# Kernel optimization log

Hardware: AMD Instinct MI355X
Metric: run time of the kernel (lower is better)

## Reference

```python
import jax, jax.numpy as jnp
import numpy as np

# model dims
C_CH = 64      # channels C
M_DIM = 128    # state dim m
R = 8          # low-rank r
DG = 64        # token_dim d_g
CHUNK = 512    # chunk_len
B, H, W = 4, 256, 256


def setup_inputs() -> dict:
    key = jax.random.key(0)
    ks = jax.random.split(key, 12)
    n = jax.random.normal
    return {
        "x": n(ks[0], (B, C_CH, H, W), jnp.float32),
        "g": n(ks[1], (B, DG), jnp.float32),
        # 1x1 conv weights flattened to matrices
        "in_proj_w": n(ks[2], (M_DIM, C_CH), jnp.float32) * 0.05,
        "in_proj_b": jnp.zeros((M_DIM,), jnp.float32),
        "out_proj_w": n(ks[3], (C_CH, M_DIM), jnp.float32) * 0.05,  # Cbase; conv bias unused in forward
        "U_base": n(ks[4], (M_DIM, R), jnp.float32) * 0.02,
        "V_base": n(ks[5], (M_DIM, R), jnp.float32) * 0.02,
        "a_base": jnp.zeros((M_DIM,), jnp.float32),
        "mod_uv_w": n(ks[6], (2 * R, DG), jnp.float32) * 0.05,
        "mod_uv_b": jnp.zeros((2 * R,), jnp.float32),
        "mod_a_w": n(ks[7], (M_DIM, DG), jnp.float32) * 0.05,
        "mod_a_b": jnp.zeros((M_DIM,), jnp.float32),
        "mod_B_w": n(ks[8], (M_DIM, DG), jnp.float32) * 0.05,
        "mod_B_b": jnp.zeros((M_DIM,), jnp.float32),
        "mod_C_w": n(ks[9], (C_CH, DG), jnp.float32) * 0.05,
        "mod_C_b": jnp.zeros((C_CH,), jnp.float32),
        "h0": jnp.zeros((M_DIM,), jnp.float32),
    }


def reference(x, g, in_proj_w, in_proj_b, out_proj_w, U_base, V_base, a_base,
              mod_uv_w, mod_uv_b, mod_a_w, mod_a_b, mod_B_w, mod_B_b,
              mod_C_w, mod_C_b, h0):
    Bsz, Cch, Hh, Ww = x.shape
    # 1x1 conv in_proj
    x_proj = jnp.einsum('bchw,mc->bmhw', x, in_proj_w) + in_proj_b[None, :, None, None]
    # g-conditioned modulations
    uv = g @ mod_uv_w.T + mod_uv_b
    gU = jnp.clip(uv[:, :R], -0.5, 0.5)[:, None, :]          # (B,1,r)
    gV = jnp.clip(uv[:, R:], -0.5, 0.5)[:, None, :]          # (B,1,r)
    ga = jnp.clip(g @ mod_a_w.T + mod_a_b, -2.0, 2.0)        # (B,m)
    gB = jnp.clip(g @ mod_B_w.T + mod_B_b, -1.0, 1.0)        # (B,m)
    gC = jnp.clip(g @ mod_C_w.T + mod_C_b, -0.5, 0.5)        # (B,C)
    Ug = U_base[None] * (1.0 + gU)                            # (B,m,r)
    Vg = V_base[None] * (1.0 + gV)                            # (B,m,r)
    a = a_base[None] + ga                                     # (B,m)
    Cg = out_proj_w[None] * (1.0 + gC)[:, :, None]            # (B,C,m)

    L = Hh * Ww
    x_seq = x_proj.reshape(Bsz, M_DIM, L).transpose(0, 2, 1)  # (B,L,m)
    x_seq = x_seq * (1.0 + gB)[:, None, :]
    pad = (-L) % CHUNK
    if pad > 0:
        x_seq = jnp.pad(x_seq, ((0, 0), (0, pad), (0, 0)))
    Lp = L + pad
    Mch = Lp // CHUNK
    # (T, B, K, m): scan over time within chunks, chunks run in parallel
    x_chunks = x_seq.reshape(Bsz, Mch, CHUNK, M_DIM).transpose(2, 0, 1, 3)
    h_init = jnp.broadcast_to(h0, (Bsz, Mch, M_DIM))

    def step(h, xt):
        v = jnp.einsum('bmr,bkm->bkr', Vg, h)                 # V^T h
        Av = jnp.einsum('bmr,bkr->bkm', Ug, v)                # U (V^T h)
        h_new = jnp.clip(Av + h * a[:, None, :] + xt, -10.0, 10.0)
        yc = jnp.clip(jnp.einsum('bcm,bkm->bkc', Cg, h_new), -10.0, 10.0)
        return h_new, yc

    _, ys = jax.lax.scan(step, h_init, x_chunks)              # (T,B,K,C)
    out_flat = ys.transpose(1, 2, 0, 3).reshape(Bsz, Lp, Cch)[:, :L, :]
    return out_flat.transpose(0, 2, 1).reshape(Bsz, Cch, Hh, Ww)
```

## Files before the change

### kernel.cpp

```cpp
#include <hip/hip_runtime.h>
#include <hip/hip_fp16.h>

#define L_TOT 65536

#define WS_UG   0
#define WS_VG   4096
#define WS_A    8192
#define WS_GB1  8704
#define WS_WHP  12288
#define WS_WLP  16384
#define WS_CGP  32768
#define WS_XS   65536

typedef __attribute__((ext_vector_type(8))) short short8;
typedef __attribute__((ext_vector_type(4))) float f32x4;

__device__ __forceinline__ unsigned bf16rne(float f) {
    unsigned u = __builtin_bit_cast(unsigned, f);
    return (u + 0x7fffu + ((u >> 16) & 1u)) >> 16;
}
__device__ __forceinline__ float bfhi(unsigned u) {
    return __builtin_bit_cast(float, u << 16);
}

#define DPP_ROW(CT) \
    "v_add_f32_dpp %0, %0, %0 " CT "\n\t" \
    "v_add_f32_dpp %1, %1, %1 " CT "\n\t" \
    "v_add_f32_dpp %2, %2, %2 " CT "\n\t" \
    "v_add_f32_dpp %3, %3, %3 " CT "\n\t" \
    "v_add_f32_dpp %4, %4, %4 " CT "\n\t" \
    "v_add_f32_dpp %5, %5, %5 " CT "\n\t" \
    "v_add_f32_dpp %6, %6, %6 " CT "\n\t" \
    "v_add_f32_dpp %7, %7, %7 " CT "\n\t"

__global__ __launch_bounds__(128) void mod_kernel(
    const float* __restrict__ g, const float* __restrict__ in_proj_w,
    const float* __restrict__ U_base, const float* __restrict__ V_base,
    const float* __restrict__ a_base, const float* __restrict__ out_proj_w,
    const float* __restrict__ mod_uv_w, const float* __restrict__ mod_uv_b,
    const float* __restrict__ mod_a_w, const float* __restrict__ mod_a_b,
    const float* __restrict__ mod_B_w, const float* __restrict__ mod_B_b,
    const float* __restrict__ mod_C_w, const float* __restrict__ mod_C_b,
    float* __restrict__ ws)
{
    __shared__ float gsh[64];
    __shared__ float uvs[16];
    __shared__ float gCs[64];
    const int b = blockIdx.x, tid = threadIdx.x;
    if (tid < 64) gsh[tid] = g[b * 64 + tid];
    __syncthreads();
    if (tid < 16) {
        float s = mod_uv_b[tid];
        for (int d = 0; d < 64; ++d) s += mod_uv_w[tid * 64 + d] * gsh[d];
        uvs[tid] = fminf(0.5f, fmaxf(-0.5f, s));
    }
    float ga_v, gB_v;
    {
        float s = mod_a_b[tid];
        for (int d = 0; d < 64; ++d) s += mod_a_w[tid * 64 + d] * gsh[d];
        ga_v = fminf(2.0f, fmaxf(-2.0f, s));
    }
    {
        float s = mod_B_b[tid];
        for (int d = 0; d < 64; ++d) s += mod_B_w[tid * 64 + d] * gsh[d];
        gB_v = 1.0f + fminf(1.0f, fmaxf(-1.0f, s));
    }
    if (tid < 64) {
        float s = mod_C_b[tid];
        for (int d = 0; d < 64; ++d) s += mod_C_w[tid * 64 + d] * gsh[d];
        gCs[tid] = 1.0f + fminf(0.5f, fmaxf(-0.5f, s));
    }
    __syncthreads();
    for (int idx = tid; idx < 1024; idx += 128) {
        int m = idx >> 3, r = idx & 7;
        ws[WS_UG + (b * 128 + m) * 8 + r] = U_base[m * 8 + r] * (1.0f + uvs[r]);
        ws[WS_VG + (b * 128 + m) * 8 + r] = V_base[m * 8 + r] * (1.0f + uvs[8 + r]);
    }
    ws[WS_A   + b * 128 + tid] = a_base[tid] + ga_v;
    ws[WS_GB1 + b * 128 + tid] = gB_v;
    unsigned* CgP = (unsigned*)(ws + WS_CGP);
    for (int idx = tid; idx < 4096; idx += 128) {
        int c = idx >> 6, j = idx & 63;
        float s = gCs[c];
        float c0 = out_proj_w[c * 128 + 2 * j]     * s;
        float c1 = out_proj_w[c * 128 + 2 * j + 1] * s;
        CgP[(b * 64 + c) * 64 + j] = bf16rne(c0) | (bf16rne(c1) << 16);
    }
    if (b == 0) {
        unsigned* WhP = (unsigned*)(ws + WS_WHP);
        unsigned* WlP = (unsigned*)(ws + WS_WLP);
        for (int idx = tid; idx < 4096; idx += 128) {
            int m = idx >> 5, j = idx & 31;
            float w0 = in_proj_w[m * 64 + 2 * j];
            float w1 = in_proj_w[m * 64 + 2 * j + 1];
            unsigned u0 = bf16rne(w0), u1 = bf16rne(w1);
            WhP[idx] = u0 | (u1 << 16);
            float r0 = w0 - bfhi(u0);
            float r1 = w1 - bfhi(u1);
            WlP[idx] = bf16rne(r0) | (bf16rne(r1) << 16);
        }
    }
}

__global__ __launch_bounds__(256) void inproj_mfma(
    const float* __restrict__ x, const unsigned* __restrict__ WhP,
    const unsigned* __restrict__ WlP, const float* __restrict__ bias,
    const float* __restrict__ ws, unsigned* __restrict__ xs16)
{
    __shared__ __align__(16) unsigned XhS[64 * 36];
    __shared__ __align__(16) unsigned XlS[64 * 36];
    const int tid = threadIdx.x;
    const int b = blockIdx.y;
    const int l0 = blockIdx.x * 64;

    {
        const int l_st = tid & 63, cpg = tid >> 6;
        #pragma unroll
        for (int s = 0; s < 8; ++s) {
            int cp = cpg * 8 + s;
            float x0 = x[(size_t)(b * 64 + 2 * cp) * L_TOT + l0 + l_st];
            float x1 = x[(size_t)(b * 64 + 2 * cp + 1) * L_TOT + l0 + l_st];
            unsigned u0 = bf16rne(x0), u1 = bf16rne(x1);
            XhS[l_st * 36 + cp] = u0 | (u1 << 16);
            float r0 = x0 - bfhi(u0);
            float r1 = x1 - bfhi(u1);
            XlS[l_st * 36 + cp] = bf16rne(r0) | (bf16rne(r1) << 16);
        }
    }
    const int lane = tid & 63, wv = tid >> 6;
    const int row16 = lane & 15, grp = lane >> 4;

    short8 Ah[2][2], Al[2][2];
    #pragma unroll
    for (int t = 0; t < 2; ++t) {
        const int mrow = (2 * wv + t) * 16 + row16;
        #pragma unroll
        for (int kc = 0; kc < 2; ++kc) {
            Ah[t][kc] = __builtin_bit_cast(short8,
                *(const uint4*)(WhP + mrow * 32 + kc * 16 + grp * 4));
            Al[t][kc] = __builtin_bit_cast(short8,
                *(const uint4*)(WlP + mrow * 32 + kc * 16 + grp * 4));
        }
    }
    __syncthreads();

    #pragma unroll
    for (int ti = 0; ti < 4; ++ti) {
        const int lcol = ti * 16 + row16;
        short8 Bh[2], Bl[2];
        #pragma unroll
        for (int kc = 0; kc < 2; ++kc) {
            Bh[kc] = __builtin_bit_cast(short8,
                *(const uint4*)&XhS[lcol * 36 + kc * 16 + grp * 4]);
            Bl[kc] = __builtin_bit_cast(short8,
                *(const uint4*)&XlS[lcol * 36 + kc * 16 + grp * 4]);
        }
        #pragma unroll
        for (int t = 0; t < 2; ++t) {
            f32x4 acc = {0.f, 0.f, 0.f, 0.f};
            acc = __builtin_amdgcn_mfma_f32_16x16x32_bf16(Ah[t][0], Bh[0], acc, 0, 0, 0);
            acc = __builtin_amdgcn_mfma_f32_16x16x32_bf16(Ah[t][1], Bh[1], acc, 0, 0, 0);
            acc = __builtin_amdgcn_mfma_f32_16x16x32_bf16(Ah[t][0], Bl[0], acc, 0, 0, 0);
            acc = __builtin_amdgcn_mfma_f32_16x16x32_bf16(Ah[t][1], Bl[1], acc, 0, 0, 0);
            acc = __builtin_amdgcn_mfma_f32_16x16x32_bf16(Al[t][0], Bh[0], acc, 0, 0, 0);
            acc = __builtin_amdgcn_mfma_f32_16x16x32_bf16(Al[t][1], Bh[1], acc, 0, 0, 0);
            const int mb = (2 * wv + t) * 16 + 4 * grp;
            const int l = l0 + lcol;
            float4 bi = *(const float4*)(bias + mb);
            float4 gb = *(const float4*)(ws + WS_GB1 + b * 128 + mb);
            float v0 = (acc[0] + bi.x) * gb.x;
            float v1 = (acc[1] + bi.y) * gb.y;
            float v2 = (acc[2] + bi.z) * gb.z;
            float v3 = (acc[3] + bi.w) * gb.w;
            __half2 h01 = __floats2half2_rn(v0, v1);
            __half2 h23 = __floats2half2_rn(v2, v3);
            uint2 pk = {__builtin_bit_cast(unsigned, h01), __builtin_bit_cast(unsigned, h23)};
            *(uint2*)(xs16 + ((size_t)b * L_TOT + l) * 64 + (mb >> 1)) = pk;
        }
    }
}

__global__ __launch_bounds__(64, 1) void scan_kernel(
    const unsigned* __restrict__ xs16, const float* __restrict__ ws,
    const unsigned* __restrict__ CgP, const float* __restrict__ h0,
    float* __restrict__ out)
{
    __shared__ __align__(16) unsigned Hs[16 * 68];
    const int lane = threadIdx.x;
    const int bb = blockIdx.x >> 7, k = blockIdx.x & 127;
    const int m0 = 2 * lane;

    float Vg0[8], Vg1[8], Ug0[8], Ug1[8];
    {
        const float* vg = ws + WS_VG + (bb * 128 + m0) * 8;
        const float* ug = ws + WS_UG + (bb * 128 + m0) * 8;
        #pragma unroll
        for (int r = 0; r < 8; ++r) {
            Vg0[r] = vg[r]; Vg1[r] = vg[8 + r];
            Ug0[r] = ug[r]; Ug1[r] = ug[8 + r];
        }
    }
    const float a0 = ws[WS_A + bb * 128 + m0];
    const float a1 = ws[WS_A + bb * 128 + m0 + 1];
    float ha = h0[m0], hb = h0[m0 + 1];

    short8 Af[4][4];
    const int row16 = lane & 15, grp = lane >> 4;
    #pragma unroll
    for (int ct = 0; ct < 4; ++ct)
        #pragma unroll
        for (int kc = 0; kc < 4; ++kc) {
            const unsigned* p = CgP + (bb * 64 + ct * 16 + row16) * 64 + kc * 16 + grp * 4;
            Af[ct][kc] = __builtin_bit_cast(short8, *(const uint4*)p);
        }

    const unsigned* xsp = xs16 + ((size_t)bb * L_TOT + (size_t)k * 512) * 64 + lane;
    float* ob[4];
    #pragma unroll
    for (int ct = 0; ct < 4; ++ct)
        ob[ct] = out + (size_t)(bb * 64 + ct * 16 + grp * 4) * L_TOT + k * 512 + row16;

    unsigned xqA[16], xqB[16];

    auto prefetch = [&](unsigned (&xq)[16], int seg) {
        const unsigned* xb = xsp + (size_t)seg * 1024;
        #pragma unroll
        for (int i = 0; i < 16; ++i) xq[i] = xb[(size_t)i * 64];
    };
    auto do_seg = [&](const unsigned (&xq)[16], int t16) {
        #pragma unroll
        for (int i = 0; i < 16; ++i) {
            const float2 xv = __half22float2(__builtin_bit_cast(__half2, xq[i]));
            float p0 = fmaf(Vg1[0], hb, Vg0[0] * ha);
            float p1 = fmaf(Vg1[1], hb, Vg0[1] * ha);
            float p2 = fmaf(Vg1[2], hb, Vg0[2] * ha);
            float p3 = fmaf(Vg1[3], hb, Vg0[3] * ha);
            float p4 = fmaf(Vg1[4], hb, Vg0[4] * ha);
            float p5 = fmaf(Vg1[5], hb, Vg0[5] * ha);
            float p6 = fmaf(Vg1[6], hb, Vg0[6] * ha);
            float p7 = fmaf(Vg1[7], hb, Vg0[7] * ha);
            asm volatile(
                "s_nop 1\n\t"
                DPP_ROW("quad_perm:[1,0,3,2] row_mask:0xf bank_mask:0xf bound_ctrl:1")
                DPP_ROW("quad_perm:[2,3,0,1] row_mask:0xf bank_mask:0xf bound_ctrl:1")
                DPP_ROW("row_half_mirror row_mask:0xf bank_mask:0xf bound_ctrl:1")
                DPP_ROW("row_mirror row_mask:0xf bank_mask:0xf bound_ctrl:1")
                DPP_ROW("row_bcast:15 row_mask:0xa bank_mask:0xf")
                DPP_ROW("row_bcast:31 row_mask:0xc bank_mask:0xf")
                : "+v"(p0), "+v"(p1), "+v"(p2), "+v"(p3),
                  "+v"(p4), "+v"(p5), "+v"(p6), "+v"(p7));
            float v0 = __builtin_bit_cast(float, __builtin_amdgcn_readlane(__builtin_bit_cast(int, p0), 63));
            float v1 = __builtin_bit_cast(float, __builtin_amdgcn_readlane(__builtin_bit_cast(int, p1), 63));
            float v2 = __builtin_bit_cast(float, __builtin_amdgcn_readlane(__builtin_bit_cast(int, p2), 63));
            float v3 = __builtin_bit_cast(float, __builtin_amdgcn_readlane(__builtin_bit_cast(int, p3), 63));
            float v4 = __builtin_bit_cast(float, __builtin_amdgcn_readlane(__builtin_bit_cast(int, p4), 63));
            float v5 = __builtin_bit_cast(float, __builtin_amdgcn_readlane(__builtin_bit_cast(int, p5), 63));
            float v6 = __builtin_bit_cast(float, __builtin_amdgcn_readlane(__builtin_bit_cast(int, p6), 63));
            float v7 = __builtin_bit_cast(float, __builtin_amdgcn_readlane(__builtin_bit_cast(int, p7), 63));
            float q0 = fmaf(v1, Ug0[1], v0 * Ug0[0]);
            float q1 = fmaf(v3, Ug0[3], v2 * Ug0[2]);
            float q2 = fmaf(v5, Ug0[5], v4 * Ug0[4]);
            float q3 = fmaf(v7, Ug0[7], v6 * Ug0[6]);
            float av0 = (q0 + q1) + (q2 + q3);
            float s0 = fmaf(v1, Ug1[1], v0 * Ug1[0]);
            float s1 = fmaf(v3, Ug1[3], v2 * Ug1[2]);
            float s2 = fmaf(v5, Ug1[5], v4 * Ug1[4]);
            float s3 = fmaf(v7, Ug1[7], v6 * Ug1[6]);
            float av1 = (s0 + s1) + (s2 + s3);
            ha = fminf(10.0f, fmaxf(-10.0f, fmaf(a0, ha, av0) + xv.x));
            hb = fminf(10.0f, fmaxf(-10.0f, fmaf(a1, hb, av1) + xv.y));
            unsigned hp;
            asm("v_cvt_pk_bf16_f32 %0, %1, %2" : "=v"(hp) : "v"(ha), "v"(hb));
            Hs[i * 68 + lane] = hp;
        }
        short8 Bf[4];
        #pragma unroll
        for (int kc = 0; kc < 4; ++kc)
            Bf[kc] = __builtin_bit_cast(short8,
                *(const uint4*)&Hs[row16 * 68 + kc * 16 + grp * 4]);
        #pragma unroll
        for (int ct = 0; ct < 4; ++ct) {
            f32x4 acc = {0.0f, 0.0f, 0.0f, 0.0f};
            #pragma unroll
            for (int kc = 0; kc < 4; ++kc)
                acc = __builtin_amdgcn_mfma_f32_16x16x32_bf16(Af[ct][kc], Bf[kc], acc, 0, 0, 0);
            #pragma unroll
            for (int r = 0; r < 4; ++r) {
                float y = fminf(10.0f, fmaxf(-10.0f, acc[r]));
                ob[ct][(size_t)r * L_TOT + t16 * 16] = y;
            }
        }
    };

    prefetch(xqA, 0);
    #pragma unroll 1
    for (int t16 = 0; t16 < 32; t16 += 2) {
        prefetch(xqB, t16 + 1);
        do_seg(xqA, t16);
        prefetch(xqA, (t16 + 2) & 31);
        do_seg(xqB, t16 + 1);
    }
}

extern "C" void kernel_launch(void* const* d_in, const int* in_sizes, int n_in,
                              void* d_out, int out_size, void* d_ws, size_t ws_size,
                              hipStream_t stream) {
    const float* x          = (const float*)d_in[0];
    const float* g          = (const float*)d_in[1];
    const float* in_proj_w  = (const float*)d_in[2];
    const float* in_proj_b  = (const float*)d_in[3];
    const float* out_proj_w = (const float*)d_in[4];
    const float* U_base     = (const float*)d_in[5];
    const float* V_base     = (const float*)d_in[6];
    const float* a_base     = (const float*)d_in[7];
    const float* mod_uv_w   = (const float*)d_in[8];
    const float* mod_uv_b   = (const float*)d_in[9];
    const float* mod_a_w    = (const float*)d_in[10];
    const float* mod_a_b    = (const float*)d_in[11];
    const float* mod_B_w    = (const float*)d_in[12];
    const float* mod_B_b    = (const float*)d_in[13];
    const float* mod_C_w    = (const float*)d_in[14];
    const float* mod_C_b    = (const float*)d_in[15];
    const float* h0         = (const float*)d_in[16];
    float* out = (float*)d_out;
    float* ws  = (float*)d_ws;
    unsigned* xs16 = (unsigned*)(ws + WS_XS);

    hipLaunchKernelGGL(mod_kernel, dim3(4), dim3(128), 0, stream,
                       g, in_proj_w, U_base, V_base, a_base, out_proj_w,
                       mod_uv_w, mod_uv_b, mod_a_w, mod_a_b,
                       mod_B_w, mod_B_b, mod_C_w, mod_C_b, ws);
    hipLaunchKernelGGL(inproj_mfma, dim3(1024, 4), dim3(256), 0, stream,
                       x, (const unsigned*)(ws + WS_WHP), (const unsigned*)(ws + WS_WLP),
                       in_proj_b, ws, xs16);
    hipLaunchKernelGGL(scan_kernel, dim3(512), dim3(64), 0, stream,
                       xs16, ws, (const unsigned*)(ws + WS_CGP), h0, out);
}
```

Before: 172.1 us.

## Restructure scan V^T h reduction with transposed DPP butterfly and switch output MFMA to fp16

The per-step reduction of V^T h is reorganised. The eight partial vectors are first combined across lanes, with each lane holding an xor-permuted slice of V and U, so a single register carries the rank components. That register is then summed across the wave with a swizzle and shuffle, and its values are redistributed via DPP instead of using six DPP stages per vector plus eight readlanes. The aim is to shorten the serial dependency chain of the recurrence, which bounds latency. Separately, the output-projection MFMA and the packing of Cg and H move from bf16 to fp16, which gains mantissa precision but has less range headroom (h is clipped to ±10, so this is fine).

```diff
diff --git a/kernel.cpp b/kernel.cpp
--- a/kernel.cpp
+++ b/kernel.cpp
@@ -14,6 +14,7 @@
 
 typedef __attribute__((ext_vector_type(8))) short short8;
 typedef __attribute__((ext_vector_type(4))) float f32x4;
+typedef _Float16 half8 __attribute__((ext_vector_type(8)));
 
 __device__ __forceinline__ unsigned bf16rne(float f) {
     unsigned u = __builtin_bit_cast(unsigned, f);
@@ -22,16 +23,10 @@
 __device__ __forceinline__ float bfhi(unsigned u) {
     return __builtin_bit_cast(float, u << 16);
 }
-
-#define DPP_ROW(CT) \
-    "v_add_f32_dpp %0, %0, %0 " CT "\n\t" \
-    "v_add_f32_dpp %1, %1, %1 " CT "\n\t" \
-    "v_add_f32_dpp %2, %2, %2 " CT "\n\t" \
-    "v_add_f32_dpp %3, %3, %3 " CT "\n\t" \
-    "v_add_f32_dpp %4, %4, %4 " CT "\n\t" \
-    "v_add_f32_dpp %5, %5, %5 " CT "\n\t" \
-    "v_add_f32_dpp %6, %6, %6 " CT "\n\t" \
-    "v_add_f32_dpp %7, %7, %7 " CT "\n\t"
+__device__ __forceinline__ unsigned f16pk(float a, float b) {
+    __half2 h = __floats2half2_rn(a, b);
+    return __builtin_bit_cast(unsigned, h);
+}
 
 __global__ __launch_bounds__(128) void mod_kernel(
     const float* __restrict__ g, const float* __restrict__ in_proj_w,
@@ -84,7 +79,7 @@
         float s = gCs[c];
         float c0 = out_proj_w[c * 128 + 2 * j]     * s;
         float c1 = out_proj_w[c * 128 + 2 * j + 1] * s;
-        CgP[(b * 64 + c) * 64 + j] = bf16rne(c0) | (bf16rne(c1) << 16);
+        CgP[(b * 64 + c) * 64 + j] = f16pk(c0, c1);
     }
     if (b == 0) {
         unsigned* WhP = (unsigned*)(ws + WS_WHP);
@@ -172,9 +167,7 @@
             float v1 = (acc[1] + bi.y) * gb.y;
             float v2 = (acc[2] + bi.z) * gb.z;
             float v3 = (acc[3] + bi.w) * gb.w;
-            __half2 h01 = __floats2half2_rn(v0, v1);
-            __half2 h23 = __floats2half2_rn(v2, v3);
-            uint2 pk = {__builtin_bit_cast(unsigned, h01), __builtin_bit_cast(unsigned, h23)};
+            uint2 pk = {f16pk(v0, v1), f16pk(v2, v3)};
             *(uint2*)(xs16 + ((size_t)b * L_TOT + l) * 64 + (mb >> 1)) = pk;
         }
     }
@@ -189,29 +182,31 @@
     const int lane = threadIdx.x;
     const int bb = blockIdx.x >> 7, k = blockIdx.x & 127;
     const int m0 = 2 * lane;
-
-    float Vg0[8], Vg1[8], Ug0[8], Ug1[8];
+    const int lp = lane & 7;
+    const int row16 = lane & 15, grp = lane >> 4;
+
+    float VgP0[8], VgP1[8], U0x[8], U1x[8];
     {
         const float* vg = ws + WS_VG + (bb * 128 + m0) * 8;
         const float* ug = ws + WS_UG + (bb * 128 + m0) * 8;
         #pragma unroll
-        for (int r = 0; r < 8; ++r) {
-            Vg0[r] = vg[r]; Vg1[r] = vg[8 + r];
-            Ug0[r] = ug[r]; Ug1[r] = ug[8 + r];
+        for (int j = 0; j < 8; ++j) {
+            int r = j ^ lp;
+            VgP0[j] = vg[r];     VgP1[j] = vg[8 + r];
+            U0x[j]  = ug[r];     U1x[j]  = ug[8 + r];
         }
     }
     const float a0 = ws[WS_A + bb * 128 + m0];
     const float a1 = ws[WS_A + bb * 128 + m0 + 1];
     float ha = h0[m0], hb = h0[m0 + 1];
 
-    short8 Af[4][4];
-    const int row16 = lane & 15, grp = lane >> 4;
+    half8 Af[4][4];
     #pragma unroll
     for (int ct = 0; ct < 4; ++ct)
         #pragma unroll
         for (int kc = 0; kc < 4; ++kc) {
             const unsigned* p = CgP + (bb * 64 + ct * 16 + row16) * 64 + kc * 16 + grp * 4;
-            Af[ct][kc] = __builtin_bit_cast(short8, *(const uint4*)p);
+            Af[ct][kc] = __builtin_bit_cast(half8, *(const uint4*)p);
         }
 
     const unsigned* xsp = xs16 + ((size_t)bb * L_TOT + (size_t)k * 512) * 64 + lane;
@@ -221,69 +216,89 @@
         ob[ct] = out + (size_t)(bb * 64 + ct * 16 + grp * 4) * L_TOT + k * 512 + row16;
 
     unsigned xqA[16], xqB[16];
-
     auto prefetch = [&](unsigned (&xq)[16], int seg) {
         const unsigned* xb = xsp + (size_t)seg * 1024;
         #pragma unroll
         for (int i = 0; i < 16; ++i) xq[i] = xb[(size_t)i * 64];
     };
+
+    const float fz = 0.0f;
+
     auto do_seg = [&](const unsigned (&xq)[16], int t16) {
         #pragma unroll
         for (int i = 0; i < 16; ++i) {
             const float2 xv = __half22float2(__builtin_bit_cast(__half2, xq[i]));
-            float p0 = fmaf(Vg1[0], hb, Vg0[0] * ha);
-            float p1 = fmaf(Vg1[1], hb, Vg0[1] * ha);
-            float p2 = fmaf(Vg1[2], hb, Vg0[2] * ha);
-            float p3 = fmaf(Vg1[3], hb, Vg0[3] * ha);
-            float p4 = fmaf(Vg1[4], hb, Vg0[4] * ha);
-            float p5 = fmaf(Vg1[5], hb, Vg0[5] * ha);
-            float p6 = fmaf(Vg1[6], hb, Vg0[6] * ha);
-            float p7 = fmaf(Vg1[7], hb, Vg0[7] * ha);
+            float p0 = fmaf(VgP1[0], hb, VgP0[0] * ha);
+            float p1 = fmaf(VgP1[1], hb, VgP0[1] * ha);
+            float p2 = fmaf(VgP1[2], hb, VgP0[2] * ha);
+            float p3 = fmaf(VgP1[3], hb, VgP0[3] * ha);
+            float p4 = fmaf(VgP1[4], hb, VgP0[4] * ha);
+            float p5 = fmaf(VgP1[5], hb, VgP0[5] * ha);
+            float p6 = fmaf(VgP1[6], hb, VgP0[6] * ha);
+            float p7 = fmaf(VgP1[7], hb, VgP0[7] * ha);
             asm volatile(
                 "s_nop 1\n\t"
-                DPP_ROW("quad_perm:[1,0,3,2] row_mask:0xf bank_mask:0xf bound_ctrl:1")
-                DPP_ROW("quad_perm:[2,3,0,1] row_mask:0xf bank_mask:0xf bound_ctrl:1")
-                DPP_ROW("row_half_mirror row_mask:0xf bank_mask:0xf bound_ctrl:1")
-                DPP_ROW("row_mirror row_mask:0xf bank_mask:0xf bound_ctrl:1")
-                DPP_ROW("row_bcast:15 row_mask:0xa bank_mask:0xf")
-                DPP_ROW("row_bcast:31 row_mask:0xc bank_mask:0xf")
+                "v_add_f32_dpp %0, %1, %0 quad_perm:[1,0,3,2] row_mask:0xf bank_mask:0xf bound_ctrl:1\n\t"
+                "v_add_f32_dpp %2, %3, %2 quad_perm:[1,0,3,2] row_mask:0xf bank_mask:0xf bound_ctrl:1\n\t"
+                "v_add_f32_dpp %5, %4, %5 quad_perm:[1,0,3,2] row_mask:0xf bank_mask:0xf bound_ctrl:1\n\t"
+                "v_add_f32_dpp %7, %6, %7 quad_perm:[1,0,3,2] row_mask:0xf bank_mask:0xf bound_ctrl:1\n\t"
+                "s_nop 1\n\t"
+                "v_add_f32_dpp %0, %2, %0 quad_perm:[2,3,0,1] row_mask:0xf bank_mask:0xf bound_ctrl:1\n\t"
+                "v_add_f32_dpp %7, %5, %7 quad_perm:[2,3,0,1] row_mask:0xf bank_mask:0xf bound_ctrl:1\n\t"
+                "s_nop 1\n\t"
+                "v_add_f32_dpp %0, %7, %0 row_half_mirror row_mask:0xf bank_mask:0xf bound_ctrl:1\n\t"
                 : "+v"(p0), "+v"(p1), "+v"(p2), "+v"(p3),
                   "+v"(p4), "+v"(p5), "+v"(p6), "+v"(p7));
-            float v0 = __builtin_bit_cast(float, __builtin_amdgcn_readlane(__builtin_bit_cast(int, p0), 63));
-            float v1 = __builtin_bit_cast(float, __builtin_amdgcn_readlane(__builtin_bit_cast(int, p1), 63));
-            float v2 = __builtin_bit_cast(float, __builtin_amdgcn_readlane(__builtin_bit_cast(int, p2), 63));
-            float v3 = __builtin_bit_cast(float, __builtin_amdgcn_readlane(__builtin_bit_cast(int, p3), 63));
-            float v4 = __builtin_bit_cast(float, __builtin_amdgcn_readlane(__builtin_bit_cast(int, p4), 63));
-            float v5 = __builtin_bit_cast(float, __builtin_amdgcn_readlane(__builtin_bit_cast(int, p5), 63));
-            float v6 = __builtin_bit_cast(float, __builtin_amdgcn_readlane(__builtin_bit_cast(int, p6), 63));
-            float v7 = __builtin_bit_cast(float, __builtin_amdgcn_readlane(__builtin_bit_cast(int, p7), 63));
-            float q0 = fmaf(v1, Ug0[1], v0 * Ug0[0]);
-            float q1 = fmaf(v3, Ug0[3], v2 * Ug0[2]);
-            float q2 = fmaf(v5, Ug0[5], v4 * Ug0[4]);
-            float q3 = fmaf(v7, Ug0[7], v6 * Ug0[6]);
-            float av0 = (q0 + q1) + (q2 + q3);
-            float s0 = fmaf(v1, Ug1[1], v0 * Ug1[0]);
-            float s1 = fmaf(v3, Ug1[3], v2 * Ug1[2]);
-            float s2 = fmaf(v5, Ug1[5], v4 * Ug1[4]);
-            float s3 = fmaf(v7, Ug1[7], v6 * Ug1[6]);
-            float av1 = (s0 + s1) + (s2 + s3);
+            p0 += __builtin_bit_cast(float, __builtin_amdgcn_ds_swizzle(
+                      __builtin_bit_cast(int, p0), 0x201F));
+            p0 += __builtin_bit_cast(float, __builtin_amdgcn_ds_swizzle(
+                      __builtin_bit_cast(int, p0), 0x401F));
+            p0 += __shfl_xor(p0, 32);
+            float vr1, vr2, vr3, vr4, vr5, vr6, vr7;
+            asm volatile(
+                "s_nop 1\n\t"
+                "v_add_f32_dpp %0, %7, %8 quad_perm:[1,0,3,2] row_mask:0xf bank_mask:0xf bound_ctrl:1\n\t"
+                "v_add_f32_dpp %1, %7, %8 quad_perm:[2,3,0,1] row_mask:0xf bank_mask:0xf bound_ctrl:1\n\t"
+                "v_add_f32_dpp %2, %7, %8 quad_perm:[3,2,1,0] row_mask:0xf bank_mask:0xf bound_ctrl:1\n\t"
+                "v_add_f32_dpp %6, %7, %8 row_half_mirror row_mask:0xf bank_mask:0xf bound_ctrl:1\n\t"
+                "s_nop 1\n\t"
+                "v_add_f32_dpp %5, %6, %8 quad_perm:[1,0,3,2] row_mask:0xf bank_mask:0xf bound_ctrl:1\n\t"
+                "v_add_f32_dpp %4, %6, %8 quad_perm:[2,3,0,1] row_mask:0xf bank_mask:0xf bound_ctrl:1\n\t"
+                "v_add_f32_dpp %3, %6, %8 quad_perm:[3,2,1,0] row_mask:0xf bank_mask:0xf bound_ctrl:1\n\t"
+                : "=&v"(vr1), "=&v"(vr2), "=&v"(vr3), "=&v"(vr4),
+                  "=&v"(vr5), "=&v"(vr6), "=&v"(vr7)
+                : "v"(p0), "v"(fz));
+            float c0 = fmaf(vr1, U0x[1], p0 * U0x[0]);
+            c0 = fmaf(vr2, U0x[2], c0);
+            c0 = fmaf(vr3, U0x[3], c0);
+            float c1 = vr4 * U0x[4];
+            c1 = fmaf(vr5, U0x[5], c1);
+            c1 = fmaf(vr6, U0x[6], c1);
+            c1 = fmaf(vr7, U0x[7], c1);
+            float av0 = c0 + c1;
+            float d0 = fmaf(vr1, U1x[1], p0 * U1x[0]);
+            d0 = fmaf(vr2, U1x[2], d0);
+            d0 = fmaf(vr3, U1x[3], d0);
+            float d1 = vr4 * U1x[4];
+            d1 = fmaf(vr5, U1x[5], d1);
+            d1 = fmaf(vr6, U1x[6], d1);
+            d1 = fmaf(vr7, U1x[7], d1);
+            float av1 = d0 + d1;
             ha = fminf(10.0f, fmaxf(-10.0f, fmaf(a0, ha, av0) + xv.x));
             hb = fminf(10.0f, fmaxf(-10.0f, fmaf(a1, hb, av1) + xv.y));
-            unsigned hp;
-            asm("v_cvt_pk_bf16_f32 %0, %1, %2" : "=v"(hp) : "v"(ha), "v"(hb));
-            Hs[i * 68 + lane] = hp;
-        }
-        short8 Bf[4];
+            Hs[i * 68 + lane] = f16pk(ha, hb);
+        }
+        half8 Bf[4];
         #pragma unroll
         for (int kc = 0; kc < 4; ++kc)
-            Bf[kc] = __builtin_bit_cast(short8,
+            Bf[kc] = __builtin_bit_cast(half8,
                 *(const uint4*)&Hs[row16 * 68 + kc * 16 + grp * 4]);
         #pragma unroll
         for (int ct = 0; ct < 4; ++ct) {
             f32x4 acc = {0.0f, 0.0f, 0.0f, 0.0f};
             #pragma unroll
             for (int kc = 0; kc < 4; ++kc)
-                acc = __builtin_amdgcn_mfma_f32_16x16x32_bf16(Af[ct][kc], Bf[kc], acc, 0, 0, 0);
+                acc = __builtin_amdgcn_mfma_f32_16x16x32_f16(Af[ct][kc], Bf[kc], acc, 0, 0, 0);
             #pragma unroll
             for (int r = 0; r < 4; ++r) {
                 float y = fminf(10.0f, fmaxf(-10.0f, acc[r]));
```

New measurement: 186.2 us. +8.2%, slower.
